# Kernel tuning notes

Hardware: AMD Instinct MI355X
Metric: run time of the kernel (lower is better)

## Reference

```python
import jax, jax.numpy as jnp
import numpy as np

NEG_SLOPE = 0.2  # PyG GATConv default leaky_relu slope


def _gat(x, src, dst, W, a_src, a_dst, b, n):
    # PyG GATConv (concat=True): h = x @ W.T reshaped to [n, H, C]
    H, C = a_src.shape
    h = (x @ W.T).reshape(n, H, C)
    e_src = (h * a_src).sum(-1)  # [n, H]
    e_dst = (h * a_dst).sum(-1)  # [n, H]
    e = jax.nn.leaky_relu(e_src[src] + e_dst[dst], NEG_SLOPE)  # [E, H]
    # scatter-softmax over incoming edges of each destination node
    m = jax.ops.segment_max(e, dst, num_segments=n)
    ee = jnp.exp(e - m[dst])
    s = jax.ops.segment_sum(ee, dst, num_segments=n)
    alpha = ee / s[dst]
    out = jax.ops.segment_sum(h[src] * alpha[:, :, None], dst, num_segments=n)
    return out.reshape(n, H * C) + b


def _forward(x, w, z, side_effects,
             lin1_w, att1_src, att1_dst, b1,
             lin2_w, att2_src, att2_dst, b2,
             lin3_w, att3_src, att3_dst, b3,
             lin4_w, att4_src, att4_dst, b4,
             x5_w, x5_b, x6_w, x6_b,
             w1_w, w1_b, w2_w, w2_b,
             z1_w, z1_b, z2_w, z2_b,
             s1_w, s1_b, s2_w, s2_b,
             edge_index, batch):
    n = x.shape[0]
    B = w.shape[0]
    loop = jnp.arange(n)
    src = jnp.concatenate([edge_index[0], loop])  # add self loops (PyG default)
    dst = jnp.concatenate([edge_index[1], loop])
    h = jax.nn.relu(_gat(x, src, dst, lin1_w, att1_src, att1_dst, b1, n))
    h = jax.nn.relu(_gat(h, src, dst, lin2_w, att2_src, att2_dst, b2, n))
    h = jax.nn.relu(_gat(h, src, dst, lin3_w, att3_src, att3_dst, b3, n))
    h = jax.nn.relu(_gat(h, src, dst, lin4_w, att4_src, att4_dst, b4, n))
    g = jax.ops.segment_max(h, batch, num_segments=B)  # global_max_pool
    g = jax.nn.relu(g @ x5_w.T + x5_b)
    g = jax.nn.relu(g @ x6_w.T + x6_b)  # dropout off (eval)
    we = jax.nn.relu(w @ w1_w.T + w1_b)
    we = jax.nn.relu(we @ w2_w.T + w2_b)
    ze = jax.nn.relu(z @ z1_w.T + z1_b)
    ze = jax.nn.relu(ze @ z2_w.T + z2_b)
    xwz = jnp.tanh(jnp.maximum(jnp.maximum(g, we), ze))
    se = jnp.tanh(jax.nn.relu(side_effects @ s1_w.T + s1_b) @ s2_w.T + s2_b)
    dv = xwz / jnp.maximum(jnp.linalg.norm(xwz, axis=1, keepdims=True), 1e-12)
    sv = se / jnp.maximum(jnp.linalg.norm(se, axis=1, keepdims=True), 1e-12)
    freq = 5.0 * (dv @ sv.T)
    return freq, dv, sv


def setup_inputs() -> dict:
    key = jax.random.key(0)
    N, E, B = 40000, 80000, 1000
    D0, D1, D2, DS, ED, H = 128, 2048, 2916, 1050, 64, 8
    ks = iter(jax.random.split(key, 64))
    def rn(shape, s=1.0):
        return jax.random.normal(next(ks), shape, jnp.float32) * np.float32(s)
    def wm(o, i):  # linear weight [out, in], glorot-ish
        return rn((o, i), 1.0 / np.sqrt(i))
    inp = {
        "x": rn((N, D0)),
        "edge_index": jax.random.randint(next(ks), (2, E), 0, N),
        "batch": (jnp.arange(N) * B) // N,  # sorted, every graph nonempty
        "w": rn((B, D1)),
        "z": rn((B, D2)),
        "side_effects": rn((750, DS)),
        "lin1_w": wm(96 * H, D0), "att1_src": rn((H, 96), 0.1), "att1_dst": rn((H, 96), 0.1), "b1": rn((96 * H,), 0.01),
        "lin2_w": wm(128 * H, 96 * H), "att2_src": rn((H, 128), 0.1), "att2_dst": rn((H, 128), 0.1), "b2": rn((128 * H,), 0.01),
        "lin3_w": wm(128 * H, 128 * H), "att3_src": rn((H, 128), 0.1), "att3_dst": rn((H, 128), 0.1), "b3": rn((128 * H,), 0.01),
        # GAT layer 4: 1024 -> 128, single head
        "lin4_w": wm(2 * ED, 128 * H), "att4_src": rn((1, 2 * ED), 0.1), "att4_dst": rn((1, 2 * ED), 0.1), "b4": rn((2 * ED,), 0.01),
        "x5_w": wm(ED, 2 * ED), "x5_b": rn((ED,), 0.01),
        "x6_w": wm(ED, ED), "x6_b": rn((ED,), 0.01),
        "w1_w": wm(D1, D1), "w1_b": rn((D1,), 0.01),
        "w2_w": wm(ED, D1), "w2_b": rn((ED,), 0.01),
        "z1_w": wm(1600, D2), "z1_b": rn((1600,), 0.01),
        "z2_w": wm(ED, 1600), "z2_b": rn((ED,), 0.01),
        "s1_w": wm(ED, DS), "s1_b": rn((ED,), 0.01),
        "s2_w": wm(ED, ED), "s2_b": rn((ED,), 0.01),
    }
    return inp


def reference(x, edge_index, batch, w, z, side_effects,
              lin1_w, att1_src, att1_dst, b1,
              lin2_w, att2_src, att2_dst, b2,
              lin3_w, att3_src, att3_dst, b3,
              lin4_w, att4_src, att4_dst, b4,
              x5_w, x5_b, x6_w, x6_b,
              w1_w, w1_b, w2_w, w2_b,
              z1_w, z1_b, z2_w, z2_b,
              s1_w, s1_b, s2_w, s2_b):
    return _forward(x, w, z, side_effects,
                    lin1_w, att1_src, att1_dst, b1,
                    lin2_w, att2_src, att2_dst, b2,
                    lin3_w, att3_src, att3_dst, b3,
                    lin4_w, att4_src, att4_dst, b4,
                    x5_w, x5_b, x6_w, x6_b,
                    w1_w, w1_b, w2_w, w2_b,
                    z1_w, z1_b, z2_w, z2_b,
                    s1_w, s1_b, s2_w, s2_b,
                    edge_index, batch)
```

## Files before the change

kernel.cpp:

```cpp
#include <hip/hip_runtime.h>
#include <hip/hip_bf16.h>
#include <math.h>

#define NEG_SLOPE 0.2f
typedef __hip_bfloat16 bf16;

typedef __bf16 bf16x8_t __attribute__((ext_vector_type(8)));
typedef float  f32x4_t  __attribute__((ext_vector_type(4)));

__device__ __forceinline__ float ld1(const float* p) { return *p; }
__device__ __forceinline__ float ld1(const bf16* p)  { return __bfloat162float(*p); }
__device__ __forceinline__ void  st1(float* p, float v) { *p = v; }
__device__ __forceinline__ void  st1(bf16* p, float v)  { *p = __float2bfloat16(v); }

union U16x8 { uint4 u4; unsigned short s[8]; };
union BF4   { uint2 u;  bf16 h[4]; };

__device__ __forceinline__ uint4 load8_bf16(const bf16* rowp, int k, int K)
{
    if (k + 8 <= K) return *reinterpret_cast<const uint4*>(rowp + k);
    U16x8 u;
    const unsigned short* rp = reinterpret_cast<const unsigned short*>(rowp);
#pragma unroll
    for (int i = 0; i < 8; ++i) u.s[i] = (k + i < K) ? rp[k + i] : 0;
    return u.u4;
}

__device__ __forceinline__ uint4 load8_bf16(const float* rowp, int k, int K)
{
    U16x8 u;
    if (k + 8 <= K) {
        float2 a = *reinterpret_cast<const float2*>(rowp + k);
        float2 b = *reinterpret_cast<const float2*>(rowp + k + 2);
        float2 c = *reinterpret_cast<const float2*>(rowp + k + 4);
        float2 d = *reinterpret_cast<const float2*>(rowp + k + 6);
        u.s[0] = __bfloat16_as_ushort(__float2bfloat16(a.x));
        u.s[1] = __bfloat16_as_ushort(__float2bfloat16(a.y));
        u.s[2] = __bfloat16_as_ushort(__float2bfloat16(b.x));
        u.s[3] = __bfloat16_as_ushort(__float2bfloat16(b.y));
        u.s[4] = __bfloat16_as_ushort(__float2bfloat16(c.x));
        u.s[5] = __bfloat16_as_ushort(__float2bfloat16(c.y));
        u.s[6] = __bfloat16_as_ushort(__float2bfloat16(d.x));
        u.s[7] = __bfloat16_as_ushort(__float2bfloat16(d.y));
    } else {
#pragma unroll
        for (int i = 0; i < 8; ++i)
            u.s[i] = (k + i < K) ? __bfloat16_as_ushort(__float2bfloat16(rowp[k + i])) : 0;
    }
    return u.u4;
}

__device__ __forceinline__ int xcd_swizzle(int orig, int nwg)
{
    const int NX = 8;
    int q = nwg / NX, r = nwg % NX;
    int xcd = orig % NX, i = orig / NX;
    return (xcd < r ? xcd * (q + 1) : r * (q + 1) + (xcd - r) * q) + i;
}

__device__ __forceinline__ void async_load16(const void* g, void* l)
{
    __builtin_amdgcn_global_load_lds(
        (const __attribute__((address_space(1))) void*)g,
        (__attribute__((address_space(3))) void*)l, 16, 0, 0);
}

template<int ACT, typename TC>
__global__ __launch_bounds__(256)
void gemm_mfma_gs(const bf16* __restrict__ A, const bf16* __restrict__ W,
                  const float* __restrict__ bias, TC* __restrict__ C,
                  int M, int N, int K, float scale)
{
    __shared__ unsigned short As[128 * 64];
    __shared__ unsigned short Bs[128 * 64];

    const int nbx = gridDim.x, nby = gridDim.y;
    const int nwg = nbx * nby;
    const int orig = blockIdx.y * nbx + blockIdx.x;
    const int wid  = xcd_swizzle(orig, nwg);
    const int brow = wid / nby;
    const int bcol = wid - brow * nby;

    const int tid  = threadIdx.x;
    const int wave = tid >> 6;
    const int lane = tid & 63;
    const int lr   = lane & 15;
    const int lg   = lane >> 4;
    const int row0 = brow * 128;
    const int col0 = bcol * 128;
    const int wm   = (wave >> 1) * 64;
    const int wn   = (wave & 1) * 64;

    const bf16* srcA[4];
    const bf16* srcB[4];
#pragma unroll
    for (int p = 0; p < 4; ++p) {
        int c = p * 256 + wave * 64 + lane;
        int m = c >> 3, s = c & 7;
        int ksw = s ^ (m & 7);
        int ra = row0 + m; ra = (ra < M) ? ra : (M - 1);
        int rb = col0 + m; rb = (rb < N) ? rb : (N - 1);
        srcA[p] = A + (size_t)ra * K + ksw * 8;
        srcB[p] = W + (size_t)rb * K + ksw * 8;
    }

    f32x4_t acc[4][4];
#pragma unroll
    for (int i = 0; i < 4; ++i)
#pragma unroll
        for (int j = 0; j < 4; ++j) acc[i][j] = (f32x4_t){0.f, 0.f, 0.f, 0.f};

    for (int k0 = 0; k0 < K; k0 += 64) {
#pragma unroll
        for (int p = 0; p < 4; ++p) {
            int base = (p * 256 + wave * 64) * 8;
            async_load16(srcA[p] + k0, &As[base]);
            async_load16(srcB[p] + k0, &Bs[base]);
        }
        __syncthreads();

#pragma unroll
        for (int ks = 0; ks < 2; ++ks) {
            bf16x8_t af[4], bfv[4];
#pragma unroll
            for (int i = 0; i < 4; ++i) {
                int row = wm + i * 16 + lr;
                int s = (ks * 4 + lg) ^ (row & 7);
                af[i] = *reinterpret_cast<const bf16x8_t*>(&As[row * 64 + s * 8]);
            }
#pragma unroll
            for (int j = 0; j < 4; ++j) {
                int row = wn + j * 16 + lr;
                int s = (ks * 4 + lg) ^ (row & 7);
                bfv[j] = *reinterpret_cast<const bf16x8_t*>(&Bs[row * 64 + s * 8]);
            }
#pragma unroll
            for (int i = 0; i < 4; ++i)
#pragma unroll
                for (int j = 0; j < 4; ++j)
                    acc[i][j] = __builtin_amdgcn_mfma_f32_16x16x32_bf16(
                        af[i], bfv[j], acc[i][j], 0, 0, 0);
        }
        __syncthreads();
    }

#pragma unroll
    for (int i = 0; i < 4; ++i) {
        int rbase = row0 + wm + i * 16 + lg * 4;
#pragma unroll
        for (int j = 0; j < 4; ++j) {
            int col = col0 + wn + j * 16 + lr;
            if (col >= N) continue;
            float bv = bias ? bias[col] : 0.f;
#pragma unroll
            for (int r = 0; r < 4; ++r) {
                int row = rbase + r;
                if (row >= M) continue;
                float v = acc[i][j][r] * scale + bv;
                if (ACT == 1) v = fmaxf(v, 0.f);
                if (ACT == 2) v = tanhf(v);
                st1(&C[(size_t)row * N + col], v);
            }
        }
    }
}

template<int ACT, typename TC>
static inline void mfma128gs(const bf16* A, const bf16* W, const float* bias, TC* C,
                             int M, int N, int K, float scale, hipStream_t st)
{
    dim3 grid((M + 127) / 128, (N + 127) / 128);
    gemm_mfma_gs<ACT, TC><<<grid, 256, 0, st>>>(A, W, bias, C, M, N, K, scale);
}

template<int ACT, typename TA, typename TW, typename TC>
__global__ __launch_bounds__(256)
void gemm_mfma(const TA* __restrict__ A, const TW* __restrict__ W,
               const float* __restrict__ bias, TC* __restrict__ C,
               int M, int N, int K, float scale)
{
    __shared__ unsigned short As[128 * 64];
    __shared__ unsigned short Bs[128 * 64];

    const int nbx = gridDim.x, nby = gridDim.y;
    const int nwg = nbx * nby;
    const int orig = blockIdx.y * nbx + blockIdx.x;
    const int wid  = xcd_swizzle(orig, nwg);
    const int brow = wid / nby;
    const int bcol = wid - brow * nby;

    const int tid  = threadIdx.x;
    const int wave = tid >> 6;
    const int lane = tid & 63;
    const int lr   = lane & 15;
    const int lg   = lane >> 4;
    const int row0 = brow * 128;
    const int col0 = bcol * 128;
    const int wm   = (wave >> 1) * 64;
    const int wn   = (wave & 1) * 64;

    f32x4_t acc[4][4];
#pragma unroll
    for (int i = 0; i < 4; ++i)
#pragma unroll
        for (int j = 0; j < 4; ++j) acc[i][j] = (f32x4_t){0.f, 0.f, 0.f, 0.f};

    uint4 va[4], vb[4];
    auto load_tiles = [&](int k0) {
#pragma unroll
        for (int p = 0; p < 4; ++p) {
            int c = tid + p * 256;
            int m = c >> 3, kc = (c & 7) * 8;
            int ra = row0 + m; ra = (ra < M) ? ra : (M - 1);
            int rb = col0 + m; rb = (rb < N) ? rb : (N - 1);
            va[p] = load8_bf16(A + (size_t)ra * K, k0 + kc, K);
            vb[p] = load8_bf16(W + (size_t)rb * K, k0 + kc, K);
        }
    };

    load_tiles(0);
    for (int k0 = 0;;) {
        __syncthreads();
#pragma unroll
        for (int p = 0; p < 4; ++p) {
            int c = tid + p * 256;
            int m = c >> 3;
            int s = (c & 7) ^ (m & 7);
            *reinterpret_cast<uint4*>(&As[m * 64 + s * 8]) = va[p];
        }
#pragma unroll
        for (int p = 0; p < 4; ++p) {
            int c = tid + p * 256;
            int m = c >> 3;
            int s = (c & 7) ^ (m & 7);
            *reinterpret_cast<uint4*>(&Bs[m * 64 + s * 8]) = vb[p];
        }
        __syncthreads();

        k0 += 64;
        const bool more = (k0 < K);
        if (more) load_tiles(k0);

#pragma unroll
        for (int ks = 0; ks < 2; ++ks) {
            bf16x8_t af[4], bfv[4];
#pragma unroll
            for (int i = 0; i < 4; ++i) {
                int row = wm + i * 16 + lr;
                int s = (ks * 4 + lg) ^ (row & 7);
                af[i] = *reinterpret_cast<const bf16x8_t*>(&As[row * 64 + s * 8]);
            }
#pragma unroll
            for (int j = 0; j < 4; ++j) {
                int row = wn + j * 16 + lr;
                int s = (ks * 4 + lg) ^ (row & 7);
                bfv[j] = *reinterpret_cast<const bf16x8_t*>(&Bs[row * 64 + s * 8]);
            }
#pragma unroll
            for (int i = 0; i < 4; ++i)
#pragma unroll
                for (int j = 0; j < 4; ++j)
                    acc[i][j] = __builtin_amdgcn_mfma_f32_16x16x32_bf16(
                        af[i], bfv[j], acc[i][j], 0, 0, 0);
        }
        if (!more) break;
    }

#pragma unroll
    for (int i = 0; i < 4; ++i) {
        int rbase = row0 + wm + i * 16 + lg * 4;
#pragma unroll
        for (int j = 0; j < 4; ++j) {
            int col = col0 + wn + j * 16 + lr;
            if (col >= N) continue;
            float bv = bias ? bias[col] : 0.f;
#pragma unroll
            for (int r = 0; r < 4; ++r) {
                int row = rbase + r;
                if (row >= M) continue;
                float v = acc[i][j][r] * scale + bv;
                if (ACT == 1) v = fmaxf(v, 0.f);
                if (ACT == 2) v = tanhf(v);
                st1(&C[(size_t)row * N + col], v);
            }
        }
    }
}

template<int ACT, typename TA, typename TW, typename TC>
static inline void mfma128(const TA* A, const TW* W, const float* bias, TC* C,
                           int M, int N, int K, float scale, hipStream_t st)
{
    dim3 grid((M + 127) / 128, (N + 127) / 128);
    gemm_mfma<ACT, TA, TW, TC><<<grid, 256, 0, st>>>(A, W, bias, C, M, N, K, scale);
}

template<typename TA, typename TW>
__global__ __launch_bounds__(256)
void gemm_mfma_sk(const TA* __restrict__ A, const TW* __restrict__ W,
                  float* __restrict__ Cp, int M, int N, int K, int Kc)
{
    __shared__ unsigned short As[128 * 64];
    __shared__ unsigned short Bs[128 * 64];

    const int tid  = threadIdx.x;
    const int wave = tid >> 6;
    const int lane = tid & 63;
    const int lr   = lane & 15;
    const int lg   = lane >> 4;
    const int row0 = blockIdx.x * 128;
    const int col0 = blockIdx.y * 128;
    const int sp   = blockIdx.z;
    const int kb   = sp * Kc;
    const int ke   = (kb + Kc < K) ? (kb + Kc) : K;
    const int wm   = (wave >> 1) * 64;
    const int wn   = (wave & 1) * 64;

    f32x4_t acc[4][4];
#pragma unroll
    for (int i = 0; i < 4; ++i)
#pragma unroll
        for (int j = 0; j < 4; ++j) acc[i][j] = (f32x4_t){0.f, 0.f, 0.f, 0.f};

    uint4 va[4], vb[4];
    auto load_tiles = [&](int k0) {
#pragma unroll
        for (int p = 0; p < 4; ++p) {
            int c = tid + p * 256;
            int m = c >> 3, kc = (c & 7) * 8;
            int ra = row0 + m; ra = (ra < M) ? ra : (M - 1);
            int rb = col0 + m; rb = (rb < N) ? rb : (N - 1);
            va[p] = load8_bf16(A + (size_t)ra * K, k0 + kc, K);
            vb[p] = load8_bf16(W + (size_t)rb * K, k0 + kc, K);
        }
    };

    if (kb < ke) {
        load_tiles(kb);
        for (int k0 = kb;;) {
            __syncthreads();
#pragma unroll
            for (int p = 0; p < 4; ++p) {
                int c = tid + p * 256;
                int m = c >> 3;
                int s = (c & 7) ^ (m & 7);
                *reinterpret_cast<uint4*>(&As[m * 64 + s * 8]) = va[p];
            }
#pragma unroll
            for (int p = 0; p < 4; ++p) {
                int c = tid + p * 256;
                int m = c >> 3;
                int s = (c & 7) ^ (m & 7);
                *reinterpret_cast<uint4*>(&Bs[m * 64 + s * 8]) = vb[p];
            }
            __syncthreads();

            k0 += 64;
            const bool more = (k0 < ke);
            if (more) load_tiles(k0);

#pragma unroll
            for (int ks = 0; ks < 2; ++ks) {
                bf16x8_t af[4], bfv[4];
#pragma unroll
                for (int i = 0; i < 4; ++i) {
                    int row = wm + i * 16 + lr;
                    int s = (ks * 4 + lg) ^ (row & 7);
                    af[i] = *reinterpret_cast<const bf16x8_t*>(&As[row * 64 + s * 8]);
                }
#pragma unroll
                for (int j = 0; j < 4; ++j) {
                    int row = wn + j * 16 + lr;
                    int s = (ks * 4 + lg) ^ (row & 7);
                    bfv[j] = *reinterpret_cast<const bf16x8_t*>(&Bs[row * 64 + s * 8]);
                }
#pragma unroll
                for (int i = 0; i < 4; ++i)
#pragma unroll
                    for (int j = 0; j < 4; ++j)
                        acc[i][j] = __builtin_amdgcn_mfma_f32_16x16x32_bf16(
                            af[i], bfv[j], acc[i][j], 0, 0, 0);
            }
            if (!more) break;
        }
    }

    float* out = Cp + (size_t)sp * M * N;
#pragma unroll
    for (int i = 0; i < 4; ++i) {
        int rbase = row0 + wm + i * 16 + lg * 4;
#pragma unroll
        for (int j = 0; j < 4; ++j) {
            int col = col0 + wn + j * 16 + lr;
            if (col >= N) continue;
#pragma unroll
            for (int r = 0; r < 4; ++r) {
                int row = rbase + r;
                if (row >= M) continue;
                out[(size_t)row * N + col] = acc[i][j][r];
            }
        }
    }
}

template<typename TO>
__global__ void sk_reduce(const float* __restrict__ Cp, const float* __restrict__ bias,
                          TO* __restrict__ out, int MN, int N, int S)
{
    int t = blockIdx.x * blockDim.x + threadIdx.x;
    if (t >= MN) return;
    float v = 0.f;
    for (int s = 0; s < S; ++s) v += Cp[(size_t)s * MN + t];
    v += bias[t % N];
    st1(&out[t], fmaxf(v, 0.f));
}

__global__ void f32_to_bf16_pad(const float* __restrict__ src, bf16* __restrict__ dst,
                                int N, int K, int Kp)
{
    int t = blockIdx.x * blockDim.x + threadIdx.x;
    if (t >= N * Kp) return;
    int n = t / Kp, k = t - n * Kp;
    float v = (k < K) ? src[(size_t)n * K + k] : 0.f;
    dst[t] = __float2bfloat16(v);
}

template<int BM,int BN,int BK,int TM,int TN,int ACT, typename TA, typename TC>
__global__ __launch_bounds__((BM/TM)*(BN/TN))
void gemm_bt(const TA* __restrict__ A, const float* __restrict__ B,
             const float* __restrict__ bias, TC* __restrict__ C,
             int M, int N, int K, float scale)
{
    constexpr int TX = BN / TN;
    constexpr int TY = BM / TM;
    constexpr int NT = TX * TY;
    constexpr int EA = BM * BK / NT;
    constexpr int EB = BN * BK / NT;
    __shared__ float As[BK][BM + 1];
    __shared__ float Bs[BK][BN + 1];

    const int tid = threadIdx.x;
    const int tx = tid % TX;
    const int ty = tid / TX;
    const int row0 = blockIdx.x * BM;
    const int col0 = blockIdx.y * BN;

    float acc[TM][TN];
#pragma unroll
    for (int i = 0; i < TM; ++i)
#pragma unroll
        for (int j = 0; j < TN; ++j) acc[i][j] = 0.f;

    for (int k0 = 0; k0 < K; k0 += BK) {
#pragma unroll
        for (int i = 0; i < EA; ++i) {
            int e = tid + i * NT;
            int m = e / BK, kk = e % BK;
            int row = row0 + m, k = k0 + kk;
            As[kk][m] = (row < M && k < K) ? ld1(&A[(size_t)row * K + k]) : 0.f;
        }
#pragma unroll
        for (int i = 0; i < EB; ++i) {
            int e = tid + i * NT;
            int c = e / BK, kk = e % BK;
            int col = col0 + c, k = k0 + kk;
            Bs[kk][c] = (col < N && k < K) ? B[(size_t)col * K + k] : 0.f;
        }
        __syncthreads();
#pragma unroll
        for (int kk = 0; kk < BK; ++kk) {
            float a[TM], b[TN];
#pragma unroll
            for (int i = 0; i < TM; ++i) a[i] = As[kk][ty + i * TY];
#pragma unroll
            for (int j = 0; j < TN; ++j) b[j] = Bs[kk][tx + j * TX];
#pragma unroll
            for (int i = 0; i < TM; ++i)
#pragma unroll
                for (int j = 0; j < TN; ++j)
                    acc[i][j] = fmaf(a[i], b[j], acc[i][j]);
        }
        __syncthreads();
    }

#pragma unroll
    for (int i = 0; i < TM; ++i) {
        int row = row0 + ty + i * TY;
        if (row >= M) continue;
#pragma unroll
        for (int j = 0; j < TN; ++j) {
            int col = col0 + tx + j * TX;
            if (col >= N) continue;
            float v = acc[i][j] * scale + (bias ? bias[col] : 0.f);
            if (ACT == 1) v = fmaxf(v, 0.f);
            if (ACT == 2) v = tanhf(v);
            st1(&C[(size_t)row * N + col], v);
        }
    }
}

template<int ACT>
static inline void gemm64(const float* A, const float* B, const float* bias, float* C,
                          int M, int N, int K, float scale, hipStream_t st)
{
    dim3 grid((M + 63) / 64, (N + 63) / 64);
    gemm_bt<64,64,16,4,4,ACT,float,float><<<grid, 256, 0, st>>>(A, B, bias, C, M, N, K, scale);
}

__global__ void zero_i32(int* __restrict__ p, int n)
{
    int t = blockIdx.x * blockDim.x + threadIdx.x;
    if (t < n) p[t] = 0;
}

__global__ void build_edges(const int* __restrict__ ei, int* __restrict__ src,
                            int* __restrict__ dst, int* __restrict__ deg,
                            int E, int n)
{
    int t = blockIdx.x * blockDim.x + threadIdx.x;
    int Etot = E + n;
    if (t >= Etot) return;
    int s, d;
    if (t < E) { s = ei[t]; d = ei[E + t]; }
    else       { s = d = t - E; }
    src[t] = s;
    dst[t] = d;
    atomicAdd(&deg[d], 1);
}

__global__ __launch_bounds__(1024)
void scan_block(const int* __restrict__ deg, int* __restrict__ rs,
                int* __restrict__ bsum, int n)
{
    __shared__ int buf[1024];
    const int t = threadIdx.x;
    const int i = blockIdx.x * 1024 + t;
    int v = (i < n) ? deg[i] : 0;
    buf[t] = v;
    __syncthreads();
    for (int off = 1; off < 1024; off <<= 1) {
        int add = (t >= off) ? buf[t - off] : 0;
        __syncthreads();
        buf[t] += add;
        __syncthreads();
    }
    if (i < n) rs[i] = buf[t] - v;
    if (t == 1023) bsum[blockIdx.x] = buf[1023];
}

__global__ void scan_bsums(int* __restrict__ bsum, int* __restrict__ rs, int nb, int n)
{
    if (threadIdx.x == 0 && blockIdx.x == 0) {
        int acc = 0;
        for (int b = 0; b < nb; ++b) { int t = bsum[b]; bsum[b] = acc; acc += t; }
        rs[n] = acc;
    }
}

__global__ void scan_add(int* __restrict__ rs, const int* __restrict__ bsum, int n)
{
    int i = blockIdx.x * blockDim.x + threadIdx.x;
    if (i < n) rs[i] += bsum[i >> 10];
}

__global__ void scatter_csr(const int* __restrict__ src, const int* __restrict__ dst,
                            const int* __restrict__ rs, int* __restrict__ cursor,
                            int* __restrict__ csr_src, int Etot)
{
    int t = blockIdx.x * blockDim.x + threadIdx.x;
    if (t >= Etot) return;
    int d = dst[t];
    int pos = atomicAdd(&cursor[d], 1);
    csr_src[rs[d] + pos] = src[t];
}

__global__ void gat_scores(const bf16* __restrict__ h, const float* __restrict__ as,
                           const float* __restrict__ ad, float* __restrict__ es,
                           float* __restrict__ edt, int C)
{
    const int i = blockIdx.x;
    const int H = blockDim.x >> 5;
    const int hh = threadIdx.x >> 5;
    const int lane = threadIdx.x & 31;
    const bf16* hr = h + ((size_t)i * H + hh) * C;
    const float* a1 = as + hh * C;
    const float* a2 = ad + hh * C;
    float ps = 0.f, pd = 0.f;
    for (int c0 = lane * 4; c0 < C; c0 += 128) {
        BF4 hv;
        hv.u = *reinterpret_cast<const uint2*>(hr + c0);
#pragma unroll
        for (int q = 0; q < 4; ++q) {
            float v = __bfloat162float(hv.h[q]);
            ps = fmaf(v, a1[c0 + q], ps);
            pd = fmaf(v, a2[c0 + q], pd);
        }
    }
#pragma unroll
    for (int o = 16; o; o >>= 1) {
        ps += __shfl_down(ps, o, 32);
        pd += __shfl_down(pd, o, 32);
    }
    if (lane == 0) {
        es[i * H + hh] = ps;
        edt[i * H + hh] = pd;
    }
}

__global__ void gat_softmax(const int* __restrict__ rs, const int* __restrict__ csrc,
                            const float* __restrict__ es, const float* __restrict__ edt,
                            float* __restrict__ alpha, float* __restrict__ inv,
                            int n, int H)
{
    int t = blockIdx.x * blockDim.x + threadIdx.x;
    if (t >= n * H) return;
    int d = t / H, hh = t - d * H;
    int s0 = rs[d], s1 = rs[d + 1];
    float ed = edt[d * H + hh];
    float m = -INFINITY;
    for (int e = s0; e < s1; ++e) {
        float v = es[csrc[e] * H + hh] + ed;
        v = (v >= 0.f) ? v : NEG_SLOPE * v;
        m = fmaxf(m, v);
    }
    float sum = 0.f;
    for (int e = s0; e < s1; ++e) {
        float v = es[csrc[e] * H + hh] + ed;
        v = (v >= 0.f) ? v : NEG_SLOPE * v;
        float x = expf(v - m);
        sum += x;
        alpha[(size_t)e * H + hh] = x;
    }
    inv[d * H + hh] = 1.f / sum;
}

__global__ void gat_aggregate(const int* __restrict__ rs, const int* __restrict__ csrc,
                              const float* __restrict__ alpha, const float* __restrict__ inv,
                              const bf16* __restrict__ h, const float* __restrict__ bias,
                              bf16* __restrict__ out, int n, int H, int C)
{
    const int O8 = H * C / 8;
    int g = blockIdx.x * blockDim.x + threadIdx.x;
    if (g >= n * O8) return;
    int d = g / O8, j8 = g - d * O8;
    int j = j8 * 8;
    int hh = j / C;
    int s0 = rs[d], s1 = rs[d + 1];
    float acc[8];
#pragma unroll
    for (int q = 0; q < 8; ++q) acc[q] = 0.f;
    for (int e = s0; e < s1; ++e) {
        float a = alpha[(size_t)e * H + hh];
        U16x8 hv;
        hv.u4 = *reinterpret_cast<const uint4*>(h + ((size_t)csrc[e] * O8 + j8) * 8);
#pragma unroll
        for (int q = 0; q < 8; ++q)
            acc[q] = fmaf(a, __bfloat162float(__ushort_as_bfloat16(hv.s[q])), acc[q]);
    }
    float iv = inv[d * H + hh];
    U16x8 ov;
#pragma unroll
    for (int q = 0; q < 8; ++q) {
        float v = fmaxf(acc[q] * iv + bias[j + q], 0.f);
        ov.s[q] = __bfloat16_as_ushort(__float2bfloat16(v));
    }
    *reinterpret_cast<uint4*>(out + ((size_t)d * O8 + j8) * 8) = ov.u4;
}

__global__ __launch_bounds__(128)
void pool_graph(const bf16* __restrict__ h, float* __restrict__ g, int n, int B)
{
    int b = blockIdx.x;
    int c = threadIdx.x;
    int i0 = (int)(((long long)b * n + B - 1) / B);
    int i1 = (int)(((long long)(b + 1) * n + B - 1) / B);
    if (i1 > n) i1 = n;
    float v = 0.f;
    for (int i = i0; i < i1; ++i)
        v = fmaxf(v, __bfloat162float(h[(size_t)i * 128 + c]));
    g[(size_t)b * 128 + c] = v;
}

__global__ void combine_dv(const float* __restrict__ g, const float* __restrict__ we,
                           const float* __restrict__ ze, float* __restrict__ dv, int rows)
{
    int row = blockIdx.x * (blockDim.x >> 6) + (threadIdx.x >> 6);
    int lane = threadIdx.x & 63;
    if (row >= rows) return;
    int idx = row * 64 + lane;
    float v = tanhf(fmaxf(fmaxf(g[idx], we[idx]), ze[idx]));
    float ss = v * v;
#pragma unroll
    for (int o = 32; o; o >>= 1) ss += __shfl_xor(ss, o);
    dv[idx] = v / fmaxf(sqrtf(ss), 1e-12f);
}

__global__ void norm_rows(const float* __restrict__ in, float* __restrict__ outp, int rows)
{
    int row = blockIdx.x * (blockDim.x >> 6) + (threadIdx.x >> 6);
    int lane = threadIdx.x & 63;
    if (row >= rows) return;
    int idx = row * 64 + lane;
    float v = in[idx];
    float ss = v * v;
#pragma unroll
    for (int o = 32; o; o >>= 1) ss += __shfl_xor(ss, o);
    outp[idx] = v / fmaxf(sqrtf(ss), 1e-12f);
}

extern "C" void kernel_launch(void* const* d_in, const int* in_sizes, int n_in,
                              void* d_out, int out_size, void* d_ws, size_t ws_size,
                              hipStream_t stream)
{
    const float* x     = (const float*)d_in[0];
    const int*   ei    = (const int*)d_in[1];
    const int*   batch = (const int*)d_in[2];
    const float* w     = (const float*)d_in[3];
    const float* z     = (const float*)d_in[4];
    const float* sef   = (const float*)d_in[5];
    (void)batch;

    const float* lin_w[4] = {(const float*)d_in[6],  (const float*)d_in[10],
                             (const float*)d_in[14], (const float*)d_in[18]};
    const float* att_s[4] = {(const float*)d_in[7],  (const float*)d_in[11],
                             (const float*)d_in[15], (const float*)d_in[19]};
    const float* att_d[4] = {(const float*)d_in[8],  (const float*)d_in[12],
                             (const float*)d_in[16], (const float*)d_in[20]};
    const float* bb[4]    = {(const float*)d_in[9],  (const float*)d_in[13],
                             (const float*)d_in[17], (const float*)d_in[21]};
    const float* x5_w = (const float*)d_in[22]; const float* x5_b = (const float*)d_in[23];
    const float* x6_w = (const float*)d_in[24]; const float* x6_b = (const float*)d_in[25];
    const float* w1_w = (const float*)d_in[26]; const float* w1_b = (const float*)d_in[27];
    const float* w2_w = (const float*)d_in[28]; const float* w2_b = (const float*)d_in[29];
    const float* z1_w = (const float*)d_in[30]; const float* z1_b = (const float*)d_in[31];
    const float* z2_w = (const float*)d_in[32]; const float* z2_b = (const float*)d_in[33];
    const float* s1_w = (const float*)d_in[34]; const float* s1_b = (const float*)d_in[35];
    const float* s2_w = (const float*)d_in[36]; const float* s2_b = (const float*)d_in[37];

    const int n    = in_sizes[0] / 128;
    const int E    = in_sizes[1] / 2;
    const int B    = in_sizes[3] / 2048;
    const int NSE  = in_sizes[5] / 1050;
    const int Etot = E + n;
    const int KZP  = 2944;
    const int NB   = (n + 1023) / 1024;

    char* ws = (char*)d_ws;
    size_t off = 0;
    auto alloc = [&](size_t bytes) -> char* {
        char* p = ws + off;
        off += (bytes + 255) & ~(size_t)255;
        return p;
    };
    int*   d_src  = (int*)alloc((size_t)Etot * 4);
    int*   d_dst  = (int*)alloc((size_t)Etot * 4);
    int*   d_deg  = (int*)alloc((size_t)n * 4);
    int*   d_rs   = (int*)alloc((size_t)(n + 1) * 4);
    int*   d_bsum = (int*)alloc((size_t)NB * 4);
    int*   d_csrc = (int*)alloc((size_t)Etot * 4);
    float* d_esrc = (float*)alloc((size_t)n * 8 * 4);
    float* d_edst = (float*)alloc((size_t)n * 8 * 4);
    float* d_inv  = (float*)alloc((size_t)n * 8 * 4);
    float* d_alp  = (float*)alloc((size_t)Etot * 8 * 4);
    bf16*  d_h    = (bf16*)alloc((size_t)n * 1024 * 2);
    bf16*  d_o    = (bf16*)alloc((size_t)n * 1024 * 2);
    bf16*  d_xb   = (bf16*)alloc((size_t)n * 128 * 2);
    bf16*  d_wb0  = (bf16*)alloc((size_t)768 * 128 * 2);
    bf16*  d_wb1  = (bf16*)alloc((size_t)1024 * 768 * 2);
    bf16*  d_wb2  = (bf16*)alloc((size_t)1024 * 1024 * 2);
    bf16*  d_wb3  = (bf16*)alloc((size_t)128 * 1024 * 2);
    bf16*  d_wB   = (bf16*)alloc((size_t)B * 2048 * 2);
    bf16*  d_zB   = (bf16*)alloc((size_t)B * KZP * 2);
    bf16*  d_w1wB = (bf16*)alloc((size_t)2048 * 2048 * 2);
    bf16*  d_z1wB = (bf16*)alloc((size_t)1600 * KZP * 2);
    float* d_g    = (float*)alloc((size_t)B * 128 * 4);
    float* d_g2   = (float*)alloc((size_t)B * 64 * 4);
    float* d_g3   = (float*)alloc((size_t)B * 64 * 4);
    bf16*  d_we1  = (bf16*)alloc((size_t)B * 2048 * 2);
    float* d_we2  = (float*)alloc((size_t)B * 64 * 4);
    bf16*  d_ze1  = (bf16*)alloc((size_t)B * 1600 * 2);
    float* d_ze2  = (float*)alloc((size_t)B * 64 * 4);
    float* d_se1  = (float*)alloc((size_t)NSE * 64 * 4);
    float* d_se2  = (float*)alloc((size_t)NSE * 64 * 4);

    if (off > ws_size) return;

    float* d_sk = (float*)d_h;

    {
        int cnt;
        cnt = n * 128;
        f32_to_bf16_pad<<<(cnt + 255) / 256, 256, 0, stream>>>(x, d_xb, n, 128, 128);
        cnt = 768 * 128;
        f32_to_bf16_pad<<<(cnt + 255) / 256, 256, 0, stream>>>(lin_w[0], d_wb0, 768, 128, 128);
        cnt = 1024 * 768;
        f32_to_bf16_pad<<<(cnt + 255) / 256, 256, 0, stream>>>(lin_w[1], d_wb1, 1024, 768, 768);
        cnt = 1024 * 1024;
        f32_to_bf16_pad<<<(cnt + 255) / 256, 256, 0, stream>>>(lin_w[2], d_wb2, 1024, 1024, 1024);
        cnt = 128 * 1024;
        f32_to_bf16_pad<<<(cnt + 255) / 256, 256, 0, stream>>>(lin_w[3], d_wb3, 128, 1024, 1024);
        cnt = B * 2048;
        f32_to_bf16_pad<<<(cnt + 255) / 256, 256, 0, stream>>>(w, d_wB, B, 2048, 2048);
        cnt = B * KZP;
        f32_to_bf16_pad<<<(cnt + 255) / 256, 256, 0, stream>>>(z, d_zB, B, 2916, KZP);
        cnt = 2048 * 2048;
        f32_to_bf16_pad<<<(cnt + 255) / 256, 256, 0, stream>>>(w1_w, d_w1wB, 2048, 2048, 2048);
        cnt = 1600 * KZP;
        f32_to_bf16_pad<<<(cnt + 255) / 256, 256, 0, stream>>>(z1_w, d_z1wB, 1600, 2916, KZP);
    }
    const bf16* wbf[4] = {d_wb0, d_wb1, d_wb2, d_wb3};

    zero_i32<<<(n + 255) / 256, 256, 0, stream>>>(d_deg, n);
    build_edges<<<(Etot + 255) / 256, 256, 0, stream>>>(ei, d_src, d_dst, d_deg, E, n);
    scan_block<<<NB, 1024, 0, stream>>>(d_deg, d_rs, d_bsum, n);
    scan_bsums<<<1, 64, 0, stream>>>(d_bsum, d_rs, NB, n);
    scan_add<<<(n + 255) / 256, 256, 0, stream>>>(d_rs, d_bsum, n);
    zero_i32<<<(n + 255) / 256, 256, 0, stream>>>(d_deg, n);
    scatter_csr<<<(Etot + 255) / 256, 256, 0, stream>>>(d_src, d_dst, d_rs, d_deg, d_csrc, Etot);

    struct LP { int I, O, H, C; };
    const LP L[4] = { {128, 768, 8, 96}, {768, 1024, 8, 128},
                      {1024, 1024, 8, 128}, {1024, 128, 1, 128} };

    mfma128gs<0>(d_xb, wbf[0], (const float*)nullptr, d_h, n, L[0].O, L[0].I, 1.f, stream);
    for (int l = 0; l < 4; ++l) {
        const int O = L[l].O, H = L[l].H, C = L[l].C;
        gat_scores<<<n, H * 32, 0, stream>>>(d_h, att_s[l], att_d[l], d_esrc, d_edst, C);
        gat_softmax<<<(n * H + 255) / 256, 256, 0, stream>>>(d_rs, d_csrc, d_esrc, d_edst,
                                                             d_alp, d_inv, n, H);
        const int O8 = O / 8;
        gat_aggregate<<<(n * O8 + 255) / 256, 256, 0, stream>>>(d_rs, d_csrc, d_alp, d_inv,
                                                                d_h, bb[l], d_o, n, H, C);
        if (l < 3)
            mfma128gs<0>(d_o, wbf[l + 1], (const float*)nullptr, d_h,
                         n, L[l + 1].O, L[l + 1].I, 1.f, stream);
    }

    pool_graph<<<B, 128, 0, stream>>>(d_o, d_g, n, B);
    mfma128<1>(d_g, x5_w, x5_b, d_g2, B, 64, 128, 1.f, stream);
    mfma128<1>(d_g2, x6_w, x6_b, d_g3, B, 64, 64, 1.f, stream);

    {
        const int S = 4, Kc = 512;
        dim3 grid((B + 127) / 128, (2048 + 127) / 128, S);
        gemm_mfma_sk<<<grid, 256, 0, stream>>>(d_wB, d_w1wB, d_sk, B, 2048, 2048, Kc);
        int MN = B * 2048;
        sk_reduce<<<(MN + 255) / 256, 256, 0, stream>>>(d_sk, w1_b, d_we1, MN, 2048, S);
    }
    {
        const int S = 8, Kc = 256;
        dim3 grid((B + 127) / 128, 1, S);
        gemm_mfma_sk<<<grid, 256, 0, stream>>>(d_we1, w2_w, d_sk, B, 64, 2048, Kc);
        int MN = B * 64;
        sk_reduce<<<(MN + 255) / 256, 256, 0, stream>>>(d_sk, w2_b, d_we2, MN, 64, S);
    }

    {
        const int S = 4, Kc = 832;
        dim3 grid((B + 127) / 128, (1600 + 127) / 128, S);
        gemm_mfma_sk<<<grid, 256, 0, stream>>>(d_zB, d_z1wB, d_sk, B, 1600, KZP, Kc);
        int MN = B * 1600;
        sk_reduce<<<(MN + 255) / 256, 256, 0, stream>>>(d_sk, z1_b, d_ze1, MN, 1600, S);
    }
    {
        const int S = 5, Kc = 320;
        dim3 grid((B + 127) / 128, 1, S);
        gemm_mfma_sk<<<grid, 256, 0, stream>>>(d_ze1, z2_w, d_sk, B, 64, 1600, Kc);
        int MN = B * 64;
        sk_reduce<<<(MN + 255) / 256, 256, 0, stream>>>(d_sk, z2_b, d_ze2, MN, 64, S);
    }

    mfma128<1>(sef, s1_w, s1_b, d_se1, NSE, 64, 1050, 1.f, stream);
    mfma128<2>(d_se1, s2_w, s2_b, d_se2, NSE, 64, 64, 1.f, stream);

    float* out   = (float*)d_out;
    float* d_dv  = out + (size_t)B * NSE;
    float* d_sv  = d_dv + (size_t)B * 64;
    combine_dv<<<(B + 3) / 4, 256, 0, stream>>>(d_g3, d_we2, d_ze2, d_dv, B);
    norm_rows<<<(NSE + 3) / 4, 256, 0, stream>>>(d_se2, d_sv, NSE);
    gemm64<0>(d_dv, d_sv, (const float*)nullptr, out, B, NSE, 64, 5.f, stream);
}
```

Measured before the change: 893.5 us.

## Fuse GAT edge softmax into aggregation and flatten score kernel grid

```diff
diff --git a/kernel.cpp b/kernel.cpp
--- a/kernel.cpp
+++ b/kernel.cpp
@@ -576,12 +576,12 @@
 
 __global__ void gat_scores(const bf16* __restrict__ h, const float* __restrict__ as,
                            const float* __restrict__ ad, float* __restrict__ es,
-                           float* __restrict__ edt, int C)
-{
-    const int i = blockIdx.x;
-    const int H = blockDim.x >> 5;
-    const int hh = threadIdx.x >> 5;
+                           float* __restrict__ edt, int n, int H, int C)
+{
+    const int grp  = (blockIdx.x * blockDim.x + threadIdx.x) >> 5;
     const int lane = threadIdx.x & 31;
+    if (grp >= n * H) return;
+    const int i = grp / H, hh = grp - i * H;
     const bf16* hr = h + ((size_t)i * H + hh) * C;
     const float* a1 = as + hh * C;
     const float* a2 = ad + hh * C;
@@ -602,40 +602,13 @@
         pd += __shfl_down(pd, o, 32);
     }
     if (lane == 0) {
-        es[i * H + hh] = ps;
-        edt[i * H + hh] = pd;
-    }
-}
-
-__global__ void gat_softmax(const int* __restrict__ rs, const int* __restrict__ csrc,
-                            const float* __restrict__ es, const float* __restrict__ edt,
-                            float* __restrict__ alpha, float* __restrict__ inv,
-                            int n, int H)
-{
-    int t = blockIdx.x * blockDim.x + threadIdx.x;
-    if (t >= n * H) return;
-    int d = t / H, hh = t - d * H;
-    int s0 = rs[d], s1 = rs[d + 1];
-    float ed = edt[d * H + hh];
-    float m = -INFINITY;
-    for (int e = s0; e < s1; ++e) {
-        float v = es[csrc[e] * H + hh] + ed;
-        v = (v >= 0.f) ? v : NEG_SLOPE * v;
-        m = fmaxf(m, v);
-    }
-    float sum = 0.f;
-    for (int e = s0; e < s1; ++e) {
-        float v = es[csrc[e] * H + hh] + ed;
-        v = (v >= 0.f) ? v : NEG_SLOPE * v;
-        float x = expf(v - m);
-        sum += x;
-        alpha[(size_t)e * H + hh] = x;
-    }
-    inv[d * H + hh] = 1.f / sum;
-}
-
-__global__ void gat_aggregate(const int* __restrict__ rs, const int* __restrict__ csrc,
-                              const float* __restrict__ alpha, const float* __restrict__ inv,
+        es[grp]  = ps;
+        edt[grp] = pd;
+    }
+}
+
+__global__ void gat_fused_agg(const int* __restrict__ rs, const int* __restrict__ csrc,
+                              const float* __restrict__ es, const float* __restrict__ edt,
                               const bf16* __restrict__ h, const float* __restrict__ bias,
                               bf16* __restrict__ out, int n, int H, int C)
 {
@@ -646,18 +619,32 @@
     int j = j8 * 8;
     int hh = j / C;
     int s0 = rs[d], s1 = rs[d + 1];
+    float ed = edt[d * H + hh];
+
+    float m = -INFINITY;
+    for (int e = s0; e < s1; ++e) {
+        float v = es[csrc[e] * H + hh] + ed;
+        v = (v >= 0.f) ? v : NEG_SLOPE * v;
+        m = fmaxf(m, v);
+    }
+
     float acc[8];
 #pragma unroll
     for (int q = 0; q < 8; ++q) acc[q] = 0.f;
+    float sum = 0.f;
     for (int e = s0; e < s1; ++e) {
-        float a = alpha[(size_t)e * H + hh];
+        int sidx = csrc[e];
+        float v = es[sidx * H + hh] + ed;
+        v = (v >= 0.f) ? v : NEG_SLOPE * v;
+        float x = expf(v - m);
+        sum += x;
         U16x8 hv;
-        hv.u4 = *reinterpret_cast<const uint4*>(h + ((size_t)csrc[e] * O8 + j8) * 8);
+        hv.u4 = *reinterpret_cast<const uint4*>(h + ((size_t)sidx * O8 + j8) * 8);
 #pragma unroll
         for (int q = 0; q < 8; ++q)
-            acc[q] = fmaf(a, __bfloat162float(__ushort_as_bfloat16(hv.s[q])), acc[q]);
-    }
-    float iv = inv[d * H + hh];
+            acc[q] = fmaf(x, __bfloat162float(__ushort_as_bfloat16(hv.s[q])), acc[q]);
+    }
+    float iv = 1.f / sum;
     U16x8 ov;
 #pragma unroll
     for (int q = 0; q < 8; ++q) {
@@ -760,8 +747,6 @@
     int*   d_csrc = (int*)alloc((size_t)Etot * 4);
     float* d_esrc = (float*)alloc((size_t)n * 8 * 4);
     float* d_edst = (float*)alloc((size_t)n * 8 * 4);
-    float* d_inv  = (float*)alloc((size_t)n * 8 * 4);
-    float* d_alp  = (float*)alloc((size_t)Etot * 8 * 4);
     bf16*  d_h    = (bf16*)alloc((size_t)n * 1024 * 2);
     bf16*  d_o    = (bf16*)alloc((size_t)n * 1024 * 2);
     bf16*  d_xb   = (bf16*)alloc((size_t)n * 128 * 2);
@@ -825,12 +810,14 @@
     mfma128gs<0>(d_xb, wbf[0], (const float*)nullptr, d_h, n, L[0].O, L[0].I, 1.f, stream);
     for (int l = 0; l < 4; ++l) {
         const int O = L[l].O, H = L[l].H, C = L[l].C;
-        gat_scores<<<n, H * 32, 0, stream>>>(d_h, att_s[l], att_d[l], d_esrc, d_edst, C);
-        gat_softmax<<<(n * H + 255) / 256, 256, 0, stream>>>(d_rs, d_csrc, d_esrc, d_edst,
-                                                             d_alp, d_inv, n, H);
+        {
+            int grps = n * H;
+            gat_scores<<<(grps * 32 + 255) / 256, 256, 0, stream>>>(
+                d_h, att_s[l], att_d[l], d_esrc, d_edst, n, H, C);
+        }
         const int O8 = O / 8;
-        gat_aggregate<<<(n * O8 + 255) / 256, 256, 0, stream>>>(d_rs, d_csrc, d_alp, d_inv,
-                                                                d_h, bb[l], d_o, n, H, C);
+        gat_fused_agg<<<(n * O8 + 255) / 256, 256, 0, stream>>>(
+            d_rs, d_csrc, d_esrc, d_edst, d_h, bb[l], d_o, n, H, C);
         if (l < 3)
             mfma128gs<0>(d_o, wbf[l + 1], (const float*)nullptr, d_h,
                          n, L[l + 1].O, L[l + 1].I, 1.f, stream);
```

Result: no change. 899.0 us (+0.6%).
